# Kernel optimization log

Measured on AMD Instinct MI355X. Metric: run time of the kernel, lower is better.

Reference implementation:

```python
import jax, jax.numpy as jnp
import numpy as np

N_IN, H1, H2, N_OUT = 1, 64, 32, 1


def _lstm_cell(x, h, c, W_ih, W_hh, b):
    # PyTorch LSTMCell gate order: i, f, g, o
    gates = x @ W_ih.T + h @ W_hh.T + b
    i, f, g, o = jnp.split(gates, 4, axis=-1)
    c_new = jax.nn.sigmoid(f) * c + jax.nn.sigmoid(i) * jnp.tanh(g)
    h_new = jax.nn.sigmoid(o) * jnp.tanh(c_new)
    return h_new, c_new


def setup_inputs() -> dict:
    key = jax.random.key(0)
    ks = jax.random.split(key, 12)
    B, T = 1024, 1024
    s1 = 1.0 / np.sqrt(H1)
    s2 = 1.0 / np.sqrt(H2)
    u = lambda k, shape, s: jax.random.uniform(k, shape, jnp.float32, -s, s)
    return {
        "input": jax.random.normal(ks[0], (B, T, N_IN), jnp.float32),
        "delayed_output": jax.random.normal(ks[1], (B, T, N_OUT), jnp.float32),
        "W_ih1": u(ks[2], (4 * H1, N_IN + N_OUT), s1),
        "W_hh1": u(ks[3], (4 * H1, H1), s1),
        "b_ih1": u(ks[4], (4 * H1,), s1),
        "b_hh1": u(ks[5], (4 * H1,), s1),
        "W_ih2": u(ks[6], (4 * H2, H1), s2),
        "W_hh2": u(ks[7], (4 * H2, H2), s2),
        "b_ih2": u(ks[8], (4 * H2,), s2),
        "b_hh2": u(ks[9], (4 * H2,), s2),
        "W_out": u(ks[10], (N_OUT, H2), s2),
        "b_out": u(ks[11], (N_OUT,), s2),
    }


def reference(input, delayed_output, W_ih1, W_hh1, b_ih1, b_hh1,
              W_ih2, W_hh2, b_ih2, b_hh2, W_out, b_out):
    B = input.shape[0]
    dt = input.dtype
    # torch.stack((input_t, delayed_output_t), 1).squeeze(-1) == concat on feature dim (n_in=n_out=1)
    feats = jnp.concatenate([input, delayed_output], axis=-1)  # [B, T, 2]
    feats = jnp.transpose(feats, (1, 0, 2))  # [T, B, 2]
    b1 = b_ih1 + b_hh1
    b2 = b_ih2 + b_hh2

    def step(carry, x_t):
        h1, c1, h2, c2 = carry
        h1, c1 = _lstm_cell(x_t, h1, c1, W_ih1, W_hh1, b1)
        h2, c2 = _lstm_cell(h1, h2, c2, W_ih2, W_hh2, b2)
        y = h2 @ W_out.T + b_out  # [B, n_out]
        return (h1, c1, h2, c2), y

    init = (jnp.zeros((B, H1), dt), jnp.zeros((B, H1), dt),
            jnp.zeros((B, H2), dt), jnp.zeros((B, H2), dt))
    _, ys = jax.lax.scan(step, init, feats)  # ys: [T, B, n_out]
    return jnp.transpose(ys, (1, 0, 2))  # [B, T, n_out]
```

## Files before the change

kernel.cpp:

```cpp
#include <hip/hip_runtime.h>


using short8 = __attribute__((ext_vector_type(8))) short;
using f32x4  = __attribute__((ext_vector_type(4))) float;
typedef unsigned short us;
typedef unsigned int   uu;

#define MFMA16(A,B,C) __builtin_amdgcn_mfma_f32_16x16x32_bf16((A),(B),(C),0,0,0)
#define BARRIER() asm volatile("s_waitcnt lgkmcnt(0)\n\ts_barrier" ::: "memory")

constexpr int   T     = 1024;
constexpr float LOG2E = 1.44269504088896f;

__device__ __forceinline__ us    bhi(float f){ return (us)(__float_as_uint(f) >> 16); }
__device__ __forceinline__ float hmask(float f){ return __uint_as_float(__float_as_uint(f) & 0xFFFF0000u); }
__device__ __forceinline__ uu rtne(float f){
    uu u = __float_as_uint(f);
    return (u + 0x7FFFu + ((u >> 16) & 1u)) >> 16;
}
__device__ __forceinline__ uu pk_bf16(float lo, float hi){
    uu r;
    asm("v_cvt_pk_bf16_f32 %0, %1, %2" : "=v"(r) : "v"(lo), "v"(hi));
    return r;
}
__device__ __forceinline__ int upos1(int p){ return 16*(p>>4) + 4*(p&3) + ((p>>2)&3); }
__device__ __forceinline__ int upos2(int p){ return 8*(p>>3) + 4*(p&1) + ((p&7)>>1); }

__device__ __forceinline__ float rcpf(float x){ return __builtin_amdgcn_rcpf(x); }
#if __has_builtin(__builtin_amdgcn_exp2f)
__device__ __forceinline__ float ex2(float x){ return __builtin_amdgcn_exp2f(x); }
#else
__device__ __forceinline__ float ex2(float x){
    float r; asm("v_exp_f32 %0, %1\n\ts_nop 0" : "=v"(r) : "v"(x)); return r;
}
#endif

__device__ __forceinline__ float actf(const f32x4 a, float& cs){
    float Ei = ex2(a[0]), Ef = ex2(a[1]), Eg = ex2(a[2]), Eo = ex2(a[3]);
    float si = rcpf(1.0f + Ei), sf = rcpf(1.0f + Ef);
    float rg = rcpf(1.0f + Eg), so = rcpf(1.0f + Eo);
    float gt2 = __builtin_fmaf(-4.0f * LOG2E, rg, 2.0f * LOG2E);
    cs = __builtin_fmaf(sf, cs, si * gt2);
    float Ec = ex2(cs);
    float tc = __builtin_fmaf(-2.0f, rcpf(1.0f + Ec), 1.0f);
    return so * tc;
}

__global__ __launch_bounds__(512, 2)
void lstm_ar_kernel(const float* __restrict__ x_in,
                    const float* __restrict__ dly_in,
                    const float* __restrict__ W_ih1, const float* __restrict__ W_hh1,
                    const float* __restrict__ b_ih1, const float* __restrict__ b_hh1,
                    const float* __restrict__ W_ih2, const float* __restrict__ W_hh2,
                    const float* __restrict__ b_ih2, const float* __restrict__ b_hh2,
                    const float* __restrict__ W_out, const float* __restrict__ b_out,
                    float* __restrict__ out)
{
    __shared__ __align__(16) us H1[2][16][72];
    __shared__ __align__(16) us H2[2][16][40];

    const int tid = threadIdx.x, w = tid >> 6, l = tid & 63;
    const int lb = l & 15, lq = l >> 4;
    const int bglob = blockIdx.x * 16 + lb;

    for (int i = tid; i < 2*16*72; i += 512) ((us*)H1)[i] = 0;
    for (int i = tid; i < 2*16*40; i += 512) ((us*)H2)[i] = 0;

    const int ty = lb & 3, du = lb >> 2;
    const float srow = (ty == 2) ? 2.0f * LOG2E : -LOG2E;
    const bool isA = (w < 4);
    const int  w2  = w & 3;

    short8 w1h[4][2], wxd[4];
    short8 w2h[2][2], whh[2], wbb[2];
    short8 wyh = {}, wyl = {};

    if (isA) {
        #pragma unroll
        for (int m = 0; m < 4; ++m) {
            const int G = ty * 64 + 16 * w + 4 * m + du;
            #pragma unroll
            for (int s = 0; s < 2; ++s)
                #pragma unroll
                for (int i = 0; i < 8; ++i) {
                    int p = 32*s + 8*lq + i;
                    float v = srow * W_hh1[G * 64 + upos1(p)];
                    w1h[m][s][i] = (short)rtne(v);
                }
            float q4 = 0.25f * srow;
            float wx = q4 * W_ih1[G*2+0], wd = q4 * W_ih1[G*2+1];
            float bb = q4 * (b_ih1[G] + b_hh1[G]);
            float wxh = hmask(wx), wdh = hmask(wd), bbh = hmask(bb);
            wxd[m] = (short8){ (short)bhi(wx), (short)bhi(wx), (short)bhi(wd),
                               (short)bhi(wd), (short)bhi(bb), (short)bhi(wx - wxh),
                               (short)bhi(wd - wdh), (short)bhi(bb - bbh) };
        }
    } else {
        #pragma unroll
        for (int j = 0; j < 2; ++j) {
            const int G2 = ty * 32 + 8 * w2 + 4 * j + du;
            #pragma unroll
            for (int s = 0; s < 2; ++s)
                #pragma unroll
                for (int i = 0; i < 8; ++i) {
                    int p = 32*s + 8*lq + i;
                    float v = srow * W_ih2[G2 * 64 + upos1(p)];
                    w2h[j][s][i] = (short)rtne(v);
                }
            #pragma unroll
            for (int i = 0; i < 8; ++i) {
                float v = srow * W_hh2[G2 * 32 + upos2(8*lq + i)];
                whh[j][i] = (short)rtne(v);
            }
            float bb = 0.25f * srow * (b_ih2[G2] + b_hh2[G2]);
            float bbh = hmask(bb);
            wbb[j] = (short8){ (short)bhi(bb), (short)bhi(bb - bbh), 0,0,0,0,0,0 };
        }
        if (w == 4) {
            #pragma unroll
            for (int i = 0; i < 8; ++i) {
                float v = (lb == 0) ? W_out[upos2(8*lq + i)] : 0.0f;
                float vh = hmask(v);
                wyh[i] = (short)bhi(v);
                wyl[i] = (short)bhi(v - vh);
            }
        }
    }
    const float bout = b_out[0];
    const short8 bB = (short8){(short)0x3F80,(short)0x3F80,0,0,0,0,0,0};
    const f32x4  Z4 = {0.f,0.f,0.f,0.f};

    const float* xp = x_in   + bglob * T;
    const float* dp = dly_in + bglob * T;
    float*       op = out    + bglob * T;

    float c1[4] = {0.f,0.f,0.f,0.f};
    float2 xc = {0,0}, dc = {0,0};
    if (isA) { xc = *(const float2*)xp; dc = *(const float2*)dp; }

    __syncthreads();

    auto STEP = [&](const int t, const int pw, const int pr,
                    const float xv, const float dv) {
        if (isA) {
            if (t < T) {
                const us* r1 = &H1[pr][lb][0];
                short8 hh0 = *(const short8*)(r1 + 8*lq);
                short8 hh1 = *(const short8*)(r1 + 32 + 8*lq);
                uu xu = __float_as_uint(xv), duu = __float_as_uint(dv);
                float xlo = xv - __uint_as_float(xu & 0xFFFF0000u);
                float dlo = dv - __uint_as_float(duu & 0xFFFF0000u);
                short8 bx;
                ((uu*)&bx)[0] = (xu >> 16)  | (__float_as_uint(xlo) & 0xFFFF0000u);
                ((uu*)&bx)[1] = (duu >> 16) | (__float_as_uint(dlo) & 0xFFFF0000u);
                ((uu*)&bx)[2] = 0x00003F80u | (xu & 0xFFFF0000u);
                ((uu*)&bx)[3] = (duu >> 16) | 0x3F800000u;

                f32x4 a[4];
                #pragma unroll
                for (int m = 0; m < 4; ++m) a[m] = MFMA16(w1h[m][0], hh0, Z4);
                #pragma unroll
                for (int m = 0; m < 4; ++m) a[m] = MFMA16(wxd[m],    bx,  a[m]);
                #pragma unroll
                for (int m = 0; m < 4; ++m) a[m] = MFMA16(w1h[m][1], hh1, a[m]);

                float hv[4];
                #pragma unroll
                for (int m = 0; m < 4; ++m) hv[m] = actf(a[m], c1[m]);

                uint2 P = { pk_bf16(hv[0], hv[1]), pk_bf16(hv[2], hv[3]) };
                *(uint2*)&H1[pw][lb][16*w + 4*lq] = P;
            }
        } else {
            short8 g0 = {};
            if (t >= 1) {
                const us* r2 = &H2[pw][lb][0];
                g0 = *(const short8*)(r2 + 8*lq);
            }
            if (w == 4 && t >= 2) {
                f32x4 yA = MFMA16(wyh, g0, Z4);
                f32x4 yB = MFMA16(wyl, g0, Z4);
                if (lq == 0) op[t-2] = yA[0] + yB[0] + bout;
            }
            if (t >= 1 && t <= T) {
                const us* r1 = &H1[pr][lb][0];
                short8 hh0 = *(const short8*)(r1 + 8*lq);
                short8 hh1 = *(const short8*)(r1 + 32 + 8*lq);

                f32x4 qA[2], qC[2];
                #pragma unroll
                for (int j = 0; j < 2; ++j) { qA[j] = MFMA16(w2h[j][0], hh0, Z4);
                                              qC[j] = MFMA16(whh[j],    g0,  Z4); }
                #pragma unroll
                for (int j = 0; j < 2; ++j)   qA[j] = MFMA16(wbb[j],    bB,  qA[j]);
                #pragma unroll
                for (int j = 0; j < 2; ++j)   qA[j] = MFMA16(w2h[j][1], hh1, qA[j]);

                float h2v[2];
                #pragma unroll
                for (int j = 0; j < 2; ++j) {
                    f32x4 g = qA[j] + qC[j];
                    h2v[j] = actf(g, c1[j]);
                }
                *(uu*)&H2[pr][lb][8*w2 + 2*lq] = pk_bf16(h2v[0], h2v[1]);
            }
        }
        BARRIER();
    };

    #pragma unroll 1
    for (int tt = 0; tt <= 512; ++tt) {
        float2 xn = xc, dn = dc;
        if (isA) {
            const int wn = (tt < 511) ? tt + 1 : 511;
            xn = *(const float2*)(xp + 2*wn);
            dn = *(const float2*)(dp + 2*wn);
        }
        STEP(2*tt,     0, 1, xc.x, dc.x);
        STEP(2*tt + 1, 1, 0, xc.y, dc.y);
        xc = xn; dc = dn;
    }
}

extern "C" void kernel_launch(void* const* d_in, const int* in_sizes, int n_in,
                              void* d_out, int out_size, void* d_ws, size_t ws_size,
                              hipStream_t stream) {
    lstm_ar_kernel<<<dim3(64), dim3(512), 0, stream>>>(
        (const float*)d_in[0],  (const float*)d_in[1],
        (const float*)d_in[2],  (const float*)d_in[3],
        (const float*)d_in[4],  (const float*)d_in[5],
        (const float*)d_in[6],  (const float*)d_in[7],
        (const float*)d_in[8],  (const float*)d_in[9],
        (const float*)d_in[10], (const float*)d_in[11],
        (float*)d_out);
}
```

Measured before the change: 596.0 us.

## Double block to 1024 threads, halving per-wave gate work in both LSTM layers

Each block now runs 16 waves instead of 8, so every wave computes half as many gate tiles: two MFMA chains per step for layer 1 and one for layer 2. The hidden-state write permutation changes to match the new wave-to-unit mapping. The aim is a shorter serial critical path per timestep in this latency-bound recurrence. In exchange, each barrier now synchronises twice as many waves, and layer-2 hidden writes become scalar 16-bit stores.

```diff
diff --git a/kernel.cpp b/kernel.cpp
--- a/kernel.cpp
+++ b/kernel.cpp
@@ -23,8 +23,7 @@
     asm("v_cvt_pk_bf16_f32 %0, %1, %2" : "=v"(r) : "v"(lo), "v"(hi));
     return r;
 }
-__device__ __forceinline__ int upos1(int p){ return 16*(p>>4) + 4*(p&3) + ((p>>2)&3); }
-__device__ __forceinline__ int upos2(int p){ return 8*(p>>3) + 4*(p&1) + ((p&7)>>1); }
+__device__ __forceinline__ int upos(int p){ return 8*(p>>3) + 4*(p&1) + ((p&7)>>1); }
 
 __device__ __forceinline__ float rcpf(float x){ return __builtin_amdgcn_rcpf(x); }
 #if __has_builtin(__builtin_amdgcn_exp2f)
@@ -46,7 +45,7 @@
     return so * tc;
 }
 
-__global__ __launch_bounds__(512, 2)
+__global__ __launch_bounds__(1024)
 void lstm_ar_kernel(const float* __restrict__ x_in,
                     const float* __restrict__ dly_in,
                     const float* __restrict__ W_ih1, const float* __restrict__ W_hh1,
@@ -63,28 +62,28 @@
     const int lb = l & 15, lq = l >> 4;
     const int bglob = blockIdx.x * 16 + lb;
 
-    for (int i = tid; i < 2*16*72; i += 512) ((us*)H1)[i] = 0;
-    for (int i = tid; i < 2*16*40; i += 512) ((us*)H2)[i] = 0;
+    for (int i = tid; i < 2*16*72; i += 1024) ((us*)H1)[i] = 0;
+    for (int i = tid; i < 2*16*40; i += 1024) ((us*)H2)[i] = 0;
 
     const int ty = lb & 3, du = lb >> 2;
     const float srow = (ty == 2) ? 2.0f * LOG2E : -LOG2E;
-    const bool isA = (w < 4);
-    const int  w2  = w & 3;
-
-    short8 w1h[4][2], wxd[4];
-    short8 w2h[2][2], whh[2], wbb[2];
+    const bool isA = (w < 8);
+    const int  w2  = w & 7;
+
+    short8 w1h[2][2], wxd[2];
+    short8 w2h[2], whh, wbb;
     short8 wyh = {}, wyl = {};
 
     if (isA) {
         #pragma unroll
-        for (int m = 0; m < 4; ++m) {
-            const int G = ty * 64 + 16 * w + 4 * m + du;
+        for (int m = 0; m < 2; ++m) {
+            const int G = ty * 64 + 8 * w + 4 * m + du;
             #pragma unroll
             for (int s = 0; s < 2; ++s)
                 #pragma unroll
                 for (int i = 0; i < 8; ++i) {
                     int p = 32*s + 8*lq + i;
-                    float v = srow * W_hh1[G * 64 + upos1(p)];
+                    float v = srow * W_hh1[G * 64 + upos(p)];
                     w1h[m][s][i] = (short)rtne(v);
                 }
             float q4 = 0.25f * srow;
@@ -96,30 +95,27 @@
                                (short)bhi(wd - wdh), (short)bhi(bb - bbh) };
         }
     } else {
+        const int G2 = ty * 32 + 4 * w2 + du;
         #pragma unroll
-        for (int j = 0; j < 2; ++j) {
-            const int G2 = ty * 32 + 8 * w2 + 4 * j + du;
-            #pragma unroll
-            for (int s = 0; s < 2; ++s)
-                #pragma unroll
-                for (int i = 0; i < 8; ++i) {
-                    int p = 32*s + 8*lq + i;
-                    float v = srow * W_ih2[G2 * 64 + upos1(p)];
-                    w2h[j][s][i] = (short)rtne(v);
-                }
+        for (int s = 0; s < 2; ++s)
             #pragma unroll
             for (int i = 0; i < 8; ++i) {
-                float v = srow * W_hh2[G2 * 32 + upos2(8*lq + i)];
-                whh[j][i] = (short)rtne(v);
-            }
-            float bb = 0.25f * srow * (b_ih2[G2] + b_hh2[G2]);
-            float bbh = hmask(bb);
-            wbb[j] = (short8){ (short)bhi(bb), (short)bhi(bb - bbh), 0,0,0,0,0,0 };
-        }
-        if (w == 4) {
+                int p = 32*s + 8*lq + i;
+                float v = srow * W_ih2[G2 * 64 + upos(p)];
+                w2h[s][i] = (short)rtne(v);
+            }
+        #pragma unroll
+        for (int i = 0; i < 8; ++i) {
+            float v = srow * W_hh2[G2 * 32 + 8*lq + i];
+            whh[i] = (short)rtne(v);
+        }
+        float bb = 0.25f * srow * (b_ih2[G2] + b_hh2[G2]);
+        float bbh = hmask(bb);
+        wbb = (short8){ (short)bhi(bb), (short)bhi(bb - bbh), 0,0,0,0,0,0 };
+        if (w == 8) {
             #pragma unroll
             for (int i = 0; i < 8; ++i) {
-                float v = (lb == 0) ? W_out[upos2(8*lq + i)] : 0.0f;
+                float v = (lb == 0) ? W_out[8*lq + i] : 0.0f;
                 float vh = hmask(v);
                 wyh[i] = (short)bhi(v);
                 wyl[i] = (short)bhi(v - vh);
@@ -134,7 +130,7 @@
     const float* dp = dly_in + bglob * T;
     float*       op = out    + bglob * T;
 
-    float c1[4] = {0.f,0.f,0.f,0.f};
+    float c1[2] = {0.f,0.f};
     float2 xc = {0,0}, dc = {0,0};
     if (isA) { xc = *(const float2*)xp; dc = *(const float2*)dp; }
 
@@ -156,20 +152,19 @@
                 ((uu*)&bx)[2] = 0x00003F80u | (xu & 0xFFFF0000u);
                 ((uu*)&bx)[3] = (duu >> 16) | 0x3F800000u;
 
-                f32x4 a[4];
-                #pragma unroll
-                for (int m = 0; m < 4; ++m) a[m] = MFMA16(w1h[m][0], hh0, Z4);
-                #pragma unroll
-                for (int m = 0; m < 4; ++m) a[m] = MFMA16(wxd[m],    bx,  a[m]);
-                #pragma unroll
-                for (int m = 0; m < 4; ++m) a[m] = MFMA16(w1h[m][1], hh1, a[m]);
-
-                float hv[4];
-                #pragma unroll
-                for (int m = 0; m < 4; ++m) hv[m] = actf(a[m], c1[m]);
-
-                uint2 P = { pk_bf16(hv[0], hv[1]), pk_bf16(hv[2], hv[3]) };
-                *(uint2*)&H1[pw][lb][16*w + 4*lq] = P;
+                f32x4 a[2];
+                #pragma unroll
+                for (int m = 0; m < 2; ++m) a[m] = MFMA16(w1h[m][0], hh0, Z4);
+                #pragma unroll
+                for (int m = 0; m < 2; ++m) a[m] = MFMA16(wxd[m],    bx,  a[m]);
+                #pragma unroll
+                for (int m = 0; m < 2; ++m) a[m] = MFMA16(w1h[m][1], hh1, a[m]);
+
+                float hv[2];
+                #pragma unroll
+                for (int m = 0; m < 2; ++m) hv[m] = actf(a[m], c1[m]);
+
+                *(uu*)&H1[pw][lb][8*w + 2*lq] = pk_bf16(hv[0], hv[1]);
             }
         } else {
             short8 g0 = {};
@@ -177,7 +172,7 @@
                 const us* r2 = &H2[pw][lb][0];
                 g0 = *(const short8*)(r2 + 8*lq);
             }
-            if (w == 4 && t >= 2) {
+            if (w == 8 && t >= 2) {
                 f32x4 yA = MFMA16(wyh, g0, Z4);
                 f32x4 yB = MFMA16(wyl, g0, Z4);
                 if (lq == 0) op[t-2] = yA[0] + yB[0] + bout;
@@ -187,22 +182,14 @@
                 short8 hh0 = *(const short8*)(r1 + 8*lq);
                 short8 hh1 = *(const short8*)(r1 + 32 + 8*lq);
 
-                f32x4 qA[2], qC[2];
-                #pragma unroll
-                for (int j = 0; j < 2; ++j) { qA[j] = MFMA16(w2h[j][0], hh0, Z4);
-                                              qC[j] = MFMA16(whh[j],    g0,  Z4); }
-                #pragma unroll
-                for (int j = 0; j < 2; ++j)   qA[j] = MFMA16(wbb[j],    bB,  qA[j]);
-                #pragma unroll
-                for (int j = 0; j < 2; ++j)   qA[j] = MFMA16(w2h[j][1], hh1, qA[j]);
-
-                float h2v[2];
-                #pragma unroll
-                for (int j = 0; j < 2; ++j) {
-                    f32x4 g = qA[j] + qC[j];
-                    h2v[j] = actf(g, c1[j]);
-                }
-                *(uu*)&H2[pr][lb][8*w2 + 2*lq] = pk_bf16(h2v[0], h2v[1]);
+                f32x4 qA = MFMA16(w2h[0], hh0, Z4);
+                f32x4 qC = MFMA16(whh,    g0,  Z4);
+                qA = MFMA16(wbb,    bB,  qA);
+                qA = MFMA16(w2h[1], hh1, qA);
+
+                f32x4 g = qA + qC;
+                float h2v = actf(g, c1[0]);
+                H2[pr][lb][4*w2 + lq] = (us)rtne(h2v);
             }
         }
         BARRIER();
@@ -225,7 +212,7 @@
 extern "C" void kernel_launch(void* const* d_in, const int* in_sizes, int n_in,
                               void* d_out, int out_size, void* d_ws, size_t ws_size,
                               hipStream_t stream) {
-    lstm_ar_kernel<<<dim3(64), dim3(512), 0, stream>>>(
+    lstm_ar_kernel<<<dim3(64), dim3(1024), 0, stream>>>(
         (const float*)d_in[0],  (const float*)d_in[1],
         (const float*)d_in[2],  (const float*)d_in[3],
         (const float*)d_in[4],  (const float*)d_in[5],
```

New measurement: 619.7 us. 1.04x slower.
